# Kernel optimization log

Measured on AMD Instinct MI355X. Metric: run time of the kernel, lower is better.

## Reference

```python
import jax, jax.numpy as jnp
import numpy as np

B, N, C, HID, NC = 8, 2000, 4096, 42, 20
THRESH = 0.5
EPS = 1e-12


def setup_inputs() -> dict:
    key = jax.random.key(0)
    ks = jax.random.split(key, 10)
    x1 = jax.random.normal(ks[0], (B, N, C), dtype=jnp.float32)
    x2 = jax.random.normal(ks[1], (B * N, 32), dtype=jnp.float32)  # unused after pooling in original
    xy = jax.random.uniform(ks[2], (B, N, 2), minval=0.0, maxval=800.0)
    wh = jax.random.uniform(ks[3], (B, N, 2), minval=20.0, maxval=300.0)
    boxes = jnp.concatenate([xy, xy + wh], axis=-1).astype(jnp.float32)  # [B,N,4] x1y1x2y2

    def lin(k, fi, fo):
        return (jax.random.normal(k, (fi, fo), jnp.float32) / np.sqrt(fi)).astype(jnp.float32)

    return {
        'x1': x1, 'x2': x2, 'boxes': boxes,
        'W_cls1': lin(ks[4], C, HID), 'b_cls1': jnp.zeros((HID,), jnp.float32),
        'W_cls2': lin(ks[5], HID, NC), 'b_cls2': jnp.zeros((NC,), jnp.float32),
        'W_det1': lin(ks[6], C, HID), 'b_det1': jnp.zeros((HID,), jnp.float32),
        'W_det2': lin(ks[7], HID, NC), 'b_det2': jnp.zeros((NC,), jnp.float32),
    }


def _pairwise_iou(b):  # b: [N,4]
    area = (b[:, 2] - b[:, 0]) * (b[:, 3] - b[:, 1])
    lt = jnp.maximum(b[:, None, :2], b[None, :, :2])
    rb = jnp.minimum(b[:, None, 2:], b[None, :, 2:])
    wh = jnp.clip(rb - lt, 0.0)
    inter = wh[..., 0] * wh[..., 1]
    union = area[:, None] + area[None, :] - inter
    return inter / jnp.maximum(union, EPS)


def _row_normalize(m):  # Kipf-style: D^-1 m, zero rows -> 0
    s = jnp.sum(m, axis=1, keepdims=True)
    inv = jnp.where(s == 0.0, 0.0, 1.0 / jnp.where(s == 0.0, 1.0, s))
    return m * inv


def _per_image(x, b, W_cls1, b_cls1, W_cls2, b_cls2, W_det1, b_det1, W_det2, b_det2):
    # adjacency graph from box IoU, thresholded at 0.5; edges are unweighted (GCNConv normalize=False)
    iou = _pairwise_iou(b)
    A_adj = (iou >= THRESH).astype(x.dtype)  # [N,N], includes diagonal (self-IoU=1)
    # similarity graph from cosine similarity of features
    sf = x / jnp.maximum(jnp.linalg.norm(x, axis=1, keepdims=True), EPS)
    sim = jnp.nan_to_num(sf @ sf.T)
    A_sim = (sim >= THRESH).astype(x.dtype)
    # features are detached + row-normalized in the original
    xn = _row_normalize(jax.lax.stop_gradient(x))
    # GCNConv(add_self_loops=False, normalize=False): out = A_bin @ (X @ W) + bias
    h = jax.nn.relu(A_adj @ (xn @ W_cls1) + b_cls1)  # dropout is identity in eval
    cls = A_adj @ (h @ W_cls2) + b_cls2
    hd = jax.nn.relu(A_sim @ (xn @ W_det1) + b_det1)
    det = A_sim @ (hd @ W_det2) + b_det2
    return cls, det  # [N,NC] each


def reference(x1, x2, boxes, W_cls1, b_cls1, W_cls2, b_cls2, W_det1, b_det1, W_det2, b_det2):
    # x2 is pooled then unused in the original forward
    cls, det = jax.vmap(_per_image, in_axes=(0, 0) + (None,) * 8)(
        x1, boxes, W_cls1, b_cls1, W_cls2, b_cls2, W_det1, b_det1, W_det2, b_det2)
    # eval-mode post-processing
    cls = jax.nn.softmax(cls, axis=-1)          # softmax over classes
    det = jax.nn.softmax(det, axis=1)           # per-image softmax over proposals (dim=0 per image)
    cls_logit = cls.reshape(B * N, NC)
    det_logit = det.reshape(B * N, NC)
    return cls_logit, det_logit
```

## Files before the change

kernel.cpp:

```cpp
#include <hip/hip_runtime.h>
#include <stdint.h>

typedef unsigned int u32;
typedef unsigned long long u64;
typedef unsigned short u16;
typedef unsigned char u8;

#define B_IMG 8
#define N_BOX 2000
#define N_PAD 2048
#define C_DIM 4096
#define HIDN 42
#define NCLS 20
#define NWRD 64
#define NPAIR 136
#define YG_STEPS 128

using f32x4 = __attribute__((ext_vector_type(4))) float;
using s16x8 = __attribute__((ext_vector_type(8))) short;

__device__ __forceinline__ u32 f2bf(float f) {
    u32 u = __float_as_uint(f);
    u += 0x7FFFu + ((u >> 16) & 1u);
    return u >> 16;
}

#define GLOAD_LDS16(g, l)                                                     \
    __builtin_amdgcn_global_load_lds(                                         \
        (const __attribute__((address_space(1))) void*)(g),                   \
        (__attribute__((address_space(3))) void*)(l), 16, 0, 0)

__global__ __launch_bounds__(256) void wt_build(const float* __restrict__ Wc,
                                                const float* __restrict__ Wd,
                                                u16* __restrict__ Wth,
                                                u16* __restrict__ Wtl) {
    int g = blockIdx.x * 256 + threadIdx.x;
    if (g >= 96 * C_DIM) return;
    int k = g & (C_DIM - 1);
    int c = g >> 12;
    float v = 0.0f;
    if (c < HIDN) v = Wc[k * HIDN + c];
    else if (c < 2 * HIDN) v = Wd[k * HIDN + (c - HIDN)];
    u32 hb = f2bf(v);
    float hf = __uint_as_float(hb << 16);
    u32 lb = f2bf(v - hf);
    Wth[g] = (u16)hb;
    Wtl[g] = (u16)lb;
}

__global__ __launch_bounds__(256) void sf_pad(u8* __restrict__ SF,
                                              float* __restrict__ NRM) {
    int row = blockIdx.x;
    int img = row / 48, n = N_BOX + row % 48;
    uint4* p = (uint4*)(SF + ((size_t)img * N_PAD + n) * C_DIM);
    uint4 z = make_uint4(0, 0, 0, 0);
    p[threadIdx.x] = z;
    if (threadIdx.x == 0) NRM[(size_t)img * N_PAD + n] = 1e9f;
}

__global__ __launch_bounds__(256) void rowstats(const float* __restrict__ x,
                                                float* __restrict__ inv_sum,
                                                u8* __restrict__ sf,
                                                float* __restrict__ nrm) {
    int r = blockIdx.x;
    int t = threadIdx.x;
    u8* sfrow = sf + (size_t)r * C_DIM;
    if (r >= N_BOX) {
        uint4 z = make_uint4(0, 0, 0, 0);
        uint4* p = (uint4*)sfrow;
        for (int i = t; i < C_DIM / 16; i += 256) p[i] = z;
        if (t == 0) nrm[r] = 1e9f;
        return;
    }
    const float4* xr = (const float4*)(x + (size_t)r * C_DIM);
    float4 v[4];
    float s = 0.0f, ss = 0.0f;
#pragma unroll
    for (int i = 0; i < 4; i++) {
        v[i] = xr[t + 256 * i];
        s += v[i].x + v[i].y + v[i].z + v[i].w;
        ss += v[i].x * v[i].x + v[i].y * v[i].y + v[i].z * v[i].z + v[i].w * v[i].w;
    }
    __shared__ float red[4][2];
#pragma unroll
    for (int off = 32; off; off >>= 1) {
        s += __shfl_down(s, off);
        ss += __shfl_down(ss, off);
    }
    int wid = t >> 6, lane = t & 63;
    if (lane == 0) { red[wid][0] = s; red[wid][1] = ss; }
    __syncthreads();
    s  = red[0][0] + red[1][0] + red[2][0] + red[3][0];
    ss = red[0][1] + red[1][1] + red[2][1] + red[3][1];
    if (t == 0) {
        inv_sum[r] = (s == 0.0f) ? 0.0f : 1.0f / s;
        nrm[r] = sqrtf(ss);
    }
    u32* sp = (u32*)sfrow;
#pragma unroll
    for (int i = 0; i < 4; i++) {
        float4 w = v[i];
        u32 pk = __builtin_amdgcn_cvt_pk_fp8_f32(4.f * w.x, 4.f * w.y, 0, false);
        pk = __builtin_amdgcn_cvt_pk_fp8_f32(4.f * w.z, 4.f * w.w, pk, true);
        sp[t + 256 * i] = pk;
    }
}

__global__ __launch_bounds__(256) void gemm_sim(const u8* __restrict__ sf_all,
                                                const float* __restrict__ nrm_all,
                                                u32* __restrict__ bits_all) {
    __shared__ __align__(16) char smem[32768];
    char* tmat = smem;

    int z = blockIdx.z;
    const u8* sf = sf_all + (size_t)z * N_PAD * C_DIM;
    const float* nrm = nrm_all + (size_t)z * N_PAD;
    u32* bits = bits_all + (size_t)z * N_PAD * NWRD;

    int p = blockIdx.x;
    int bi = (int)((sqrtf(8.0f * p + 1.0f) - 1.0f) * 0.5f);
    while (bi * (bi + 1) / 2 > p) bi--;
    while ((bi + 1) * (bi + 2) / 2 <= p) bi++;
    int bj = p - bi * (bi + 1) / 2;

    int t = threadIdx.x;
    int lane = t & 63;
    int w = t >> 6;
    int wm = w >> 1, wn = w & 1;
    int tr0 = bi * 128, tc0 = bj * 128;
    f32x4 acc[4][4] = {};
    int q = lane & 15, g = lane >> 4;
    int swz = (q >> 1) & 3;
    int g8 = (g & 1) * 8, gh = g >> 1;

    auto stage = [&](int it, int b) {
        int k0 = it * 64;
        u8* As = (u8*)smem + b * 16384;
        u8* Bs = As + 8192;
#pragma unroll
        for (int i = 0; i < 2; i++) {
            int ci = t + 256 * i;
            int r = ci >> 2, c16 = ci & 3;
            int sc16 = c16 ^ ((r >> 1) & 3);
            GLOAD_LDS16(sf + ((size_t)(tr0 + r) << 12) + k0 + sc16 * 16,
                        As + ci * 16);
            GLOAD_LDS16(sf + ((size_t)(tc0 + r) << 12) + k0 + sc16 * 16,
                        Bs + ci * 16);
        }
    };

    stage(0, 0);
    __syncthreads();
    for (int it = 0; it < 64; ++it) {
        int cur = it & 1;
        if (it + 1 < 64) stage(it + 1, cur ^ 1);
        const u8* As = (const u8*)smem + cur * 16384;
        const u8* Bs = As + 8192;
#pragma unroll
        for (int kk = 0; kk < 2; kk++) {
            int boff = ((2 * kk + gh) ^ swz) * 16 + g8;
            long long a[4], b[4];
#pragma unroll
            for (int m = 0; m < 4; m++)
                a[m] = *(const long long*)(As + (wm * 64 + m * 16 + q) * 64 + boff);
#pragma unroll
            for (int n = 0; n < 4; n++)
                b[n] = *(const long long*)(Bs + (wn * 64 + n * 16 + q) * 64 + boff);
#pragma unroll
            for (int m = 0; m < 4; m++)
#pragma unroll
                for (int n = 0; n < 4; n++)
                    acc[m][n] = __builtin_amdgcn_mfma_f32_16x16x32_fp8_fp8(a[m], b[n], acc[m][n], 0, 0, 0);
        }
        __syncthreads();
    }

    float ncol[4];
#pragma unroll
    for (int n = 0; n < 4; n++) ncol[n] = nrm[tc0 + wn * 64 + n * 16 + q];
#pragma unroll
    for (int m = 0; m < 4; m++)
#pragma unroll
        for (int j = 0; j < 4; j++) {
            int row = wm * 64 + m * 16 + g * 4 + j;
            float thr8 = 8.0f * nrm[tr0 + row];
#pragma unroll
            for (int n = 0; n < 4; n++) {
                int col = wn * 64 + n * 16 + q;
                tmat[row * 132 + col] = (acc[m][n][j] >= thr8 * ncol[n]) ? 1 : 0;
            }
        }
    __syncthreads();

    for (int rr = 0; rr < 32; rr++) {
        int row = w * 32 + rr;
#pragma unroll
        for (int h = 0; h < 2; h++) {
            u64 b = __ballot(tmat[row * 132 + h * 64 + lane] != 0);
            if (lane < 2)
                bits[(size_t)(tr0 + row) * NWRD + bj * 4 + 2 * h + lane] = (u32)(b >> (32 * lane));
        }
    }
    if (bi != bj) {
        for (int rr = 0; rr < 32; rr++) {
            int c = w * 32 + rr;
#pragma unroll
            for (int h = 0; h < 2; h++) {
                u64 b = __ballot(tmat[(h * 64 + lane) * 132 + c] != 0);
                if (lane < 2)
                    bits[(size_t)(tc0 + c) * NWRD + bi * 4 + 2 * h + lane] = (u32)(b >> (32 * lane));
            }
        }
    }
}

__global__ __launch_bounds__(256) void iou_bits(const float* __restrict__ boxes,
                                                u32* __restrict__ bits) {
    __shared__ float bx[N_BOX * 4];
    int blk = blockIdx.x;
    int img = blk / 500;
    int r0 = (blk % 500) * 4;
    const float* bb = boxes + (size_t)img * N_BOX * 4;
    for (int i = threadIdx.x; i < N_BOX * 4; i += 256) bx[i] = bb[i];
    __syncthreads();
    int t = threadIdx.x;
    int ri = r0 + (t >> 6);
    int wi = t & 63;
    float x1a = bx[ri * 4 + 0], y1a = bx[ri * 4 + 1];
    float x2a = bx[ri * 4 + 2], y2a = bx[ri * 4 + 3];
    float areaA = __fmul_rn(__fsub_rn(x2a, x1a), __fsub_rn(y2a, y1a));
    u32 wv = 0;
    int jb = wi * 32;
#pragma unroll 4
    for (int s = 0; s < 32; s++) {
        int j = jb + s;
        if (j < N_BOX) {
            float x1b = bx[j * 4 + 0], y1b = bx[j * 4 + 1];
            float x2b = bx[j * 4 + 2], y2b = bx[j * 4 + 3];
            float areaB = __fmul_rn(__fsub_rn(x2b, x1b), __fsub_rn(y2b, y1b));
            float ltx = fmaxf(x1a, x1b), lty = fmaxf(y1a, y1b);
            float rbx = fminf(x2a, x2b), rby = fminf(y2a, y2b);
            float wx = fmaxf(__fsub_rn(rbx, ltx), 0.0f);
            float wy = fmaxf(__fsub_rn(rby, lty), 0.0f);
            float inter = __fmul_rn(wx, wy);
            float uni = __fsub_rn(__fadd_rn(areaA, areaB), inter);
            float iou = __fdiv_rn(inter, fmaxf(uni, 1e-12f));
            if (iou >= 0.5f) wv |= (1u << s);
        }
    }
    bits[((size_t)img * N_PAD + ri) * NWRD + wi] = wv;
}

__global__ __launch_bounds__(256) void ygemm_fused(const float* __restrict__ x,
                                                   const u16* __restrict__ Wh,
                                                   const u16* __restrict__ Wl,
                                                   const float* __restrict__ INV,
                                                   u8* __restrict__ SF,
                                                   float* __restrict__ NRM,
                                                   float* __restrict__ Y,
                                                   int emit) {
    __shared__ u16 Ah[2][32 * 32];
    __shared__ u16 Al[2][32 * 32];
    __shared__ u16 Bh[2][96 * 32];
    __shared__ u16 Bl[2][96 * 32];
    __shared__ float invLds[32];

    int t = threadIdx.x;
    int row0 = blockIdx.x * 32;
    int ar = t >> 3;
    int grow = row0 + ar;
    int img = grow / N_BOX, nrow = grow - img * N_BOX;
    size_t sf_off = ((size_t)img * N_PAD + nrow) * C_DIM + (t & 7) * 4;
    const float* xrow = x + (size_t)grow * C_DIM + (t & 7) * 4;

    int w = t >> 6, lane = t & 63;
    int q = lane & 15, g = lane >> 4;
    int wr = (w & 1) * 16, wc = (w >> 1) * 48;

    f32x4 acc[3] = {};
    float sum = 0.0f, ssq = 0.0f;

    auto stage_B = [&](int sstep, int b) {
        int ks = sstep * 32;
#pragma unroll
        for (int i = 0; i < 3; i++) {
            int idx = t + 256 * i;
            int half = idx >= 384;
            int loc = half ? idx - 384 : idx;
            int cr = loc >> 2, kc2 = loc & 3;
            const u16* src = (half ? Wl : Wh) + (size_t)cr * C_DIM + ks + kc2 * 8;
            u16* dst = (half ? Bl[b] : Bh[b]) + loc * 8;
            GLOAD_LDS16(src, dst);
        }
    };

    float4 pa = *(const float4*)(xrow);
    stage_B(0, 0);

    for (int s = 0; s < YG_STEPS; ++s) {
        int buf = s & 1;
        {
            float e[4] = {pa.x, pa.y, pa.z, pa.w};
            if (emit) {
                sum += e[0] + e[1] + e[2] + e[3];
                ssq += e[0] * e[0] + e[1] * e[1] + e[2] * e[2] + e[3] * e[3];
                u32 pk = __builtin_amdgcn_cvt_pk_fp8_f32(4.f * e[0], 4.f * e[1], 0, false);
                pk = __builtin_amdgcn_cvt_pk_fp8_f32(4.f * e[2], 4.f * e[3], pk, true);
                *(u32*)(SF + sf_off + (size_t)s * 32) = pk;
            }
            u32 hb[4], lb[4];
#pragma unroll
            for (int j = 0; j < 4; j++) {
                hb[j] = f2bf(e[j]);
                float hf = __uint_as_float(hb[j] << 16);
                lb[j] = f2bf(e[j] - hf);
            }
            *(uint2*)&Ah[buf][t * 4] = make_uint2(hb[0] | (hb[1] << 16), hb[2] | (hb[3] << 16));
            *(uint2*)&Al[buf][t * 4] = make_uint2(lb[0] | (lb[1] << 16), lb[2] | (lb[3] << 16));
        }
        __syncthreads();
        if (s + 1 < YG_STEPS) {
            stage_B(s + 1, buf ^ 1);
            pa = *(const float4*)(xrow + (s + 1) * 32);
        }
        s16x8 fah, fal, fbh[3], fbl[3];
        fah = *(const s16x8*)&Ah[buf][(wr + q) * 32 + g * 8];
        fal = *(const s16x8*)&Al[buf][(wr + q) * 32 + g * 8];
#pragma unroll
        for (int n = 0; n < 3; n++) {
            fbh[n] = *(const s16x8*)&Bh[buf][(wc + n * 16 + q) * 32 + g * 8];
            fbl[n] = *(const s16x8*)&Bl[buf][(wc + n * 16 + q) * 32 + g * 8];
        }
#pragma unroll
        for (int n = 0; n < 3; n++) {
            acc[n] = __builtin_amdgcn_mfma_f32_16x16x32_bf16(fah, fbh[n], acc[n], 0, 0, 0);
            acc[n] = __builtin_amdgcn_mfma_f32_16x16x32_bf16(fal, fbh[n], acc[n], 0, 0, 0);
            acc[n] = __builtin_amdgcn_mfma_f32_16x16x32_bf16(fah, fbl[n], acc[n], 0, 0, 0);
        }
    }

    if (emit) {
        sum += __shfl_xor(sum, 1); sum += __shfl_xor(sum, 2); sum += __shfl_xor(sum, 4);
        ssq += __shfl_xor(ssq, 1); ssq += __shfl_xor(ssq, 2); ssq += __shfl_xor(ssq, 4);
        if ((t & 7) == 0) {
            invLds[ar] = (sum == 0.0f) ? 0.0f : 1.0f / sum;
            NRM[(size_t)img * N_PAD + nrow] = sqrtf(ssq);
        }
    } else {
        if ((t & 7) == 0) invLds[ar] = INV[grow];
    }
    __syncthreads();

#pragma unroll
    for (int n = 0; n < 3; n++)
#pragma unroll
        for (int j = 0; j < 4; j++) {
            int lr = wr + g * 4 + j;
            int c = wc + n * 16 + q;
            Y[(size_t)(row0 + lr) * 96 + c] = acc[n][j] * invLds[lr];
        }
}

__global__ __launch_bounds__(256) void spmm1(const u32* __restrict__ Aadj,
                                             const u32* __restrict__ Asim,
                                             const float* __restrict__ Y,
                                             const float* __restrict__ bc1,
                                             const float* __restrict__ bd1,
                                             float* __restrict__ H) {
    int gw = blockIdx.x * 4 + (threadIdx.x >> 6);
    int lane = threadIdx.x & 63;
    if (lane >= HIDN) return;
    int i = gw >> 1, br = gw & 1;
    int img = i / N_BOX, n = i % N_BOX;
    const u32* bp = (br ? Asim : Aadj) + ((size_t)img * N_PAD + n) * NWRD;
    const float* Yb = Y + (size_t)img * N_BOX * 96 + br * HIDN + lane;
    float acc = 0.0f;
    for (int w8 = 0; w8 < NWRD; w8++) {
        u32 wv = bp[w8];
        while (wv) {
            int s = __builtin_ctz(wv);
            wv &= wv - 1;
            acc += Yb[(size_t)(w8 * 32 + s) * 96];
        }
    }
    float bias = br ? bd1[lane] : bc1[lane];
    H[(size_t)i * 96 + br * HIDN + lane] = fmaxf(acc + bias, 0.0f);
}

__global__ __launch_bounds__(256) void gemm2(const float* __restrict__ H,
                                             const float* __restrict__ Wc2,
                                             const float* __restrict__ Wd2,
                                             float* __restrict__ Z) {
    __shared__ float w2[2 * HIDN * NCLS];
    for (int idx = threadIdx.x; idx < 2 * HIDN * NCLS; idx += 256) {
        int br = idx / (HIDN * NCLS), e = idx % (HIDN * NCLS);
        w2[idx] = br ? Wd2[e] : Wc2[e];
    }
    __syncthreads();
    int gidx = blockIdx.x * 256 + threadIdx.x;
    if (gidx >= 16000 * 40) return;
    int i = gidx / 40, rem = gidx % 40;
    int br = rem / NCLS, c2 = rem % NCLS;
    const float* hrow = H + (size_t)i * 96 + br * HIDN;
    const float* wp = w2 + br * HIDN * NCLS;
    float acc = 0.0f;
#pragma unroll
    for (int h = 0; h < HIDN; h++) acc += hrow[h] * wp[h * NCLS + c2];
    Z[gidx] = acc;
}

__global__ __launch_bounds__(256) void spmm2(const u32* __restrict__ Aadj,
                                             const u32* __restrict__ Asim,
                                             const float* __restrict__ Z,
                                             const float* __restrict__ bc2,
                                             const float* __restrict__ bd2,
                                             float* __restrict__ out) {
    int gw = blockIdx.x * 4 + (threadIdx.x >> 6);
    int lane = threadIdx.x & 63;
    if (lane >= NCLS) return;
    int i = gw >> 1, br = gw & 1;
    int img = i / N_BOX, n = i % N_BOX;
    const u32* bp = (br ? Asim : Aadj) + ((size_t)img * N_PAD + n) * NWRD;
    const float* Zb = Z + (size_t)img * N_BOX * 40 + br * NCLS + lane;
    float acc = 0.0f;
    for (int w8 = 0; w8 < NWRD; w8++) {
        u32 wv = bp[w8];
        while (wv) {
            int s = __builtin_ctz(wv);
            wv &= wv - 1;
            acc += Zb[(size_t)(w8 * 32 + s) * 40];
        }
    }
    float logit = acc + (br ? bd2[lane] : bc2[lane]);
    out[(br ? 320000 : 0) + (size_t)i * NCLS + lane] = logit;
}

__global__ __launch_bounds__(256) void softmax_cls(float* __restrict__ out) {
    int i = blockIdx.x * 256 + threadIdx.x;
    if (i >= 16000) return;
    float* p = out + (size_t)i * NCLS;
    float m = p[0];
#pragma unroll
    for (int c = 1; c < NCLS; c++) m = fmaxf(m, p[c]);
    float e[NCLS], s = 0.0f;
#pragma unroll
    for (int c = 0; c < NCLS; c++) { e[c] = expf(p[c] - m); s += e[c]; }
    float inv = 1.0f / s;
#pragma unroll
    for (int c = 0; c < NCLS; c++) p[c] = e[c] * inv;
}

__global__ __launch_bounds__(256) void softmax_det(float* __restrict__ out) {
    __shared__ float vals[N_BOX];
    __shared__ float redm[4];
    __shared__ float reds[4];
    int img = blockIdx.x / NCLS, c = blockIdx.x % NCLS;
    float* base = out + 320000 + (size_t)img * N_BOX * NCLS + c;
    int t = threadIdx.x;
    float m = -3.4e38f;
    for (int n = t; n < N_BOX; n += 256) {
        float v = base[(size_t)n * NCLS];
        vals[n] = v;
        m = fmaxf(m, v);
    }
#pragma unroll
    for (int off = 32; off; off >>= 1) m = fmaxf(m, __shfl_down(m, off));
    if ((t & 63) == 0) redm[t >> 6] = m;
    __syncthreads();
    m = fmaxf(fmaxf(redm[0], redm[1]), fmaxf(redm[2], redm[3]));
    float s = 0.0f;
    for (int n = t; n < N_BOX; n += 256) s += expf(vals[n] - m);
#pragma unroll
    for (int off = 32; off; off >>= 1) s += __shfl_down(s, off);
    if ((t & 63) == 0) reds[t >> 6] = s;
    __syncthreads();
    s = reds[0] + reds[1] + reds[2] + reds[3];
    float inv = 1.0f / s;
    for (int n = t; n < N_BOX; n += 256) base[(size_t)n * NCLS] = expf(vals[n] - m) * inv;
}

extern "C" void kernel_launch(void* const* d_in, const int* in_sizes, int n_in,
                              void* d_out, int out_size, void* d_ws, size_t ws_size,
                              hipStream_t stream) {
    const float* x1    = (const float*)d_in[0];
    const float* boxes = (const float*)d_in[2];
    const float* W_cls1 = (const float*)d_in[3];
    const float* b_cls1 = (const float*)d_in[4];
    const float* W_cls2 = (const float*)d_in[5];
    const float* b_cls2 = (const float*)d_in[6];
    const float* W_det1 = (const float*)d_in[7];
    const float* b_det1 = (const float*)d_in[8];
    const float* W_det2 = (const float*)d_in[9];
    const float* b_det2 = (const float*)d_in[10];
    float* out = (float*)d_out;

    char* ws = (char*)d_ws;
    size_t off = 0;
    auto alloc = [&](size_t bytes) -> void* {
        void* p = ws + off;
        off = (off + bytes + 255) & ~(size_t)255;
        return p;
    };
    u16* WTH   = (u16*)alloc((size_t)96 * C_DIM * 2);
    u16* WTL   = (u16*)alloc((size_t)96 * C_DIM * 2);
    float* INV = (float*)alloc((size_t)16000 * 4);
    float* NRM = (float*)alloc((size_t)B_IMG * N_PAD * 4);
    u32* AADJ  = (u32*)alloc((size_t)B_IMG * N_PAD * NWRD * 4);
    u32* ASIM  = (u32*)alloc((size_t)B_IMG * N_PAD * NWRD * 4);
    float* Y   = (float*)alloc((size_t)16000 * 96 * 4);
    float* H   = (float*)alloc((size_t)16000 * 96 * 4);
    float* Z   = (float*)alloc((size_t)16000 * 40 * 4);
    size_t base_need = off;
    size_t sf_full = (size_t)B_IMG * N_PAD * C_DIM;
    bool full = (ws_size >= base_need + sf_full);
    u8* SF = (u8*)alloc(full ? sf_full : (size_t)N_PAD * C_DIM);

    wt_build<<<dim3(1536), dim3(256), 0, stream>>>(W_cls1, W_det1, WTH, WTL);
    iou_bits<<<dim3(B_IMG * 500), dim3(256), 0, stream>>>(boxes, AADJ);

    if (full) {
        sf_pad<<<dim3(B_IMG * 48), dim3(256), 0, stream>>>(SF, NRM);
        ygemm_fused<<<dim3(500), dim3(256), 0, stream>>>(x1, WTH, WTL, INV, SF, NRM, Y, 1);
        gemm_sim<<<dim3(NPAIR, 1, B_IMG), dim3(256), 0, stream>>>(SF, NRM, ASIM);
    } else {
        for (int b = 0; b < B_IMG; b++) {
            rowstats<<<dim3(N_PAD), dim3(256), 0, stream>>>(
                x1 + (size_t)b * N_BOX * C_DIM, INV + (size_t)b * N_BOX, SF,
                NRM + (size_t)b * N_PAD);
            gemm_sim<<<dim3(NPAIR, 1, 1), dim3(256), 0, stream>>>(
                SF, NRM + (size_t)b * N_PAD, ASIM + (size_t)b * N_PAD * NWRD);
        }
        ygemm_fused<<<dim3(500), dim3(256), 0, stream>>>(x1, WTH, WTL, INV, SF, NRM, Y, 0);
    }

    spmm1<<<dim3(8000), dim3(256), 0, stream>>>(AADJ, ASIM, Y, b_cls1, b_det1, H);
    gemm2<<<dim3(2500), dim3(256), 0, stream>>>(H, W_cls2, W_det2, Z);
    spmm2<<<dim3(8000), dim3(256), 0, stream>>>(AADJ, ASIM, Z, b_cls2, b_det2, out);
    softmax_cls<<<dim3(63), dim3(256), 0, stream>>>(out);
    softmax_det<<<dim3(160), dim3(256), 0, stream>>>(out);
    (void)in_sizes; (void)n_in; (void)out_size; (void)d_in; (void)ws_size;
}
```

Before: 536.2 us.

## Rewrite ygemm as single-wave blocks with register-prefetched operands, no LDS

The Y = X·W GEMM kernel is restructured from 256-thread blocks that stage A and B through double-buffered LDS with a barrier each step into 64-thread single-wave blocks, each computing 16 rows by all 96 columns. The A fragments are converted to bf16 hi/lo directly in registers from global loads that are prefetched four steps ahead. The W fragments are loaded straight from global memory into registers with one-step double buffering. This removes the LDS traffic and __syncthreads and deepens the x-load pipeline, at the cost of much higher register pressure and every wave re-reading W from L2 instead of sharing it through LDS.

```diff
diff --git a/kernel.cpp b/kernel.cpp
--- a/kernel.cpp
+++ b/kernel.cpp
@@ -251,114 +251,100 @@
     bits[((size_t)img * N_PAD + ri) * NWRD + wi] = wv;
 }
 
-__global__ __launch_bounds__(256) void ygemm_fused(const float* __restrict__ x,
-                                                   const u16* __restrict__ Wh,
-                                                   const u16* __restrict__ Wl,
-                                                   const float* __restrict__ INV,
-                                                   u8* __restrict__ SF,
-                                                   float* __restrict__ NRM,
-                                                   float* __restrict__ Y,
-                                                   int emit) {
-    __shared__ u16 Ah[2][32 * 32];
-    __shared__ u16 Al[2][32 * 32];
-    __shared__ u16 Bh[2][96 * 32];
-    __shared__ u16 Bl[2][96 * 32];
-    __shared__ float invLds[32];
-
-    int t = threadIdx.x;
-    int row0 = blockIdx.x * 32;
-    int ar = t >> 3;
-    int grow = row0 + ar;
+#define YG_LOADW(ks, WH_, WL_)                                                \
+    _Pragma("unroll")                                                         \
+    for (int n = 0; n < 6; n++) {                                             \
+        int col = n * 16 + q;                                                 \
+        WH_[n] = *(const s16x8*)(Wh + (size_t)col * C_DIM + (ks) + g * 8);    \
+        WL_[n] = *(const s16x8*)(Wl + (size_t)col * C_DIM + (ks) + g * 8);    \
+    }
+
+#define YG_STEP(sidx, d, CH, CL, NH, NL)                                      \
+    {                                                                         \
+        int s_ = (sidx);                                                      \
+        if (s_ + 1 < YG_STEPS) { YG_LOADW((s_ + 1) * 32, NH, NL) }            \
+        float4 a0 = xa[d][0], a1 = xa[d][1];                                  \
+        if (s_ + 4 < YG_STEPS) {                                              \
+            xa[d][0] = *(const float4*)(xp + (s_ + 4) * 32);                  \
+            xa[d][1] = *(const float4*)(xp + (s_ + 4) * 32 + 4);              \
+        }                                                                     \
+        float e[8] = {a0.x, a0.y, a0.z, a0.w, a1.x, a1.y, a1.z, a1.w};        \
+        if (emit) {                                                           \
+            sum += e[0] + e[1] + e[2] + e[3] + e[4] + e[5] + e[6] + e[7];     \
+            ssq += e[0]*e[0] + e[1]*e[1] + e[2]*e[2] + e[3]*e[3] +            \
+                   e[4]*e[4] + e[5]*e[5] + e[6]*e[6] + e[7]*e[7];             \
+            u32 lo = __builtin_amdgcn_cvt_pk_fp8_f32(4.f*e[0], 4.f*e[1], 0, false); \
+            lo = __builtin_amdgcn_cvt_pk_fp8_f32(4.f*e[2], 4.f*e[3], lo, true);     \
+            u32 hi = __builtin_amdgcn_cvt_pk_fp8_f32(4.f*e[4], 4.f*e[5], 0, false); \
+            hi = __builtin_amdgcn_cvt_pk_fp8_f32(4.f*e[6], 4.f*e[7], hi, true);     \
+            *(uint2*)(sfp + (size_t)s_ * 32) = make_uint2(lo, hi);            \
+        }                                                                     \
+        s16x8 fah, fal;                                                       \
+        _Pragma("unroll")                                                     \
+        for (int j2 = 0; j2 < 8; j2++) {                                      \
+            u32 hb = f2bf(e[j2]);                                             \
+            float hf = __uint_as_float(hb << 16);                             \
+            fah[j2] = (short)hb;                                              \
+            fal[j2] = (short)f2bf(e[j2] - hf);                                \
+        }                                                                     \
+        _Pragma("unroll")                                                     \
+        for (int n = 0; n < 6; n++) {                                         \
+            acc[n] = __builtin_amdgcn_mfma_f32_16x16x32_bf16(fah, CH[n], acc[n], 0, 0, 0); \
+            acc[n] = __builtin_amdgcn_mfma_f32_16x16x32_bf16(fal, CH[n], acc[n], 0, 0, 0); \
+            acc[n] = __builtin_amdgcn_mfma_f32_16x16x32_bf16(fah, CL[n], acc[n], 0, 0, 0); \
+        }                                                                     \
+    }
+
+__global__ __launch_bounds__(64) void ygemm_fused(const float* __restrict__ x,
+                                                  const u16* __restrict__ Wh,
+                                                  const u16* __restrict__ Wl,
+                                                  const float* __restrict__ INV,
+                                                  u8* __restrict__ SF,
+                                                  float* __restrict__ NRM,
+                                                  float* __restrict__ Y,
+                                                  int emit) {
+    int lane = threadIdx.x;
+    int q = lane & 15, g = lane >> 4;
+    int row0 = blockIdx.x * 16;
+    int grow = row0 + q;
     int img = grow / N_BOX, nrow = grow - img * N_BOX;
-    size_t sf_off = ((size_t)img * N_PAD + nrow) * C_DIM + (t & 7) * 4;
-    const float* xrow = x + (size_t)grow * C_DIM + (t & 7) * 4;
-
-    int w = t >> 6, lane = t & 63;
-    int q = lane & 15, g = lane >> 4;
-    int wr = (w & 1) * 16, wc = (w >> 1) * 48;
-
-    f32x4 acc[3] = {};
+    const float* xp = x + (size_t)grow * C_DIM + g * 8;
+    u8* sfp = SF + ((size_t)img * N_PAD + nrow) * C_DIM + g * 8;
+
+    f32x4 acc[6] = {};
     float sum = 0.0f, ssq = 0.0f;
 
-    auto stage_B = [&](int sstep, int b) {
-        int ks = sstep * 32;
-#pragma unroll
-        for (int i = 0; i < 3; i++) {
-            int idx = t + 256 * i;
-            int half = idx >= 384;
-            int loc = half ? idx - 384 : idx;
-            int cr = loc >> 2, kc2 = loc & 3;
-            const u16* src = (half ? Wl : Wh) + (size_t)cr * C_DIM + ks + kc2 * 8;
-            u16* dst = (half ? Bl[b] : Bh[b]) + loc * 8;
-            GLOAD_LDS16(src, dst);
-        }
-    };
-
-    float4 pa = *(const float4*)(xrow);
-    stage_B(0, 0);
-
-    for (int s = 0; s < YG_STEPS; ++s) {
-        int buf = s & 1;
-        {
-            float e[4] = {pa.x, pa.y, pa.z, pa.w};
-            if (emit) {
-                sum += e[0] + e[1] + e[2] + e[3];
-                ssq += e[0] * e[0] + e[1] * e[1] + e[2] * e[2] + e[3] * e[3];
-                u32 pk = __builtin_amdgcn_cvt_pk_fp8_f32(4.f * e[0], 4.f * e[1], 0, false);
-                pk = __builtin_amdgcn_cvt_pk_fp8_f32(4.f * e[2], 4.f * e[3], pk, true);
-                *(u32*)(SF + sf_off + (size_t)s * 32) = pk;
-            }
-            u32 hb[4], lb[4];
-#pragma unroll
-            for (int j = 0; j < 4; j++) {
-                hb[j] = f2bf(e[j]);
-                float hf = __uint_as_float(hb[j] << 16);
-                lb[j] = f2bf(e[j] - hf);
-            }
-            *(uint2*)&Ah[buf][t * 4] = make_uint2(hb[0] | (hb[1] << 16), hb[2] | (hb[3] << 16));
-            *(uint2*)&Al[buf][t * 4] = make_uint2(lb[0] | (lb[1] << 16), lb[2] | (lb[3] << 16));
-        }
-        __syncthreads();
-        if (s + 1 < YG_STEPS) {
-            stage_B(s + 1, buf ^ 1);
-            pa = *(const float4*)(xrow + (s + 1) * 32);
-        }
-        s16x8 fah, fal, fbh[3], fbl[3];
-        fah = *(const s16x8*)&Ah[buf][(wr + q) * 32 + g * 8];
-        fal = *(const s16x8*)&Al[buf][(wr + q) * 32 + g * 8];
-#pragma unroll
-        for (int n = 0; n < 3; n++) {
-            fbh[n] = *(const s16x8*)&Bh[buf][(wc + n * 16 + q) * 32 + g * 8];
-            fbl[n] = *(const s16x8*)&Bl[buf][(wc + n * 16 + q) * 32 + g * 8];
-        }
-#pragma unroll
-        for (int n = 0; n < 3; n++) {
-            acc[n] = __builtin_amdgcn_mfma_f32_16x16x32_bf16(fah, fbh[n], acc[n], 0, 0, 0);
-            acc[n] = __builtin_amdgcn_mfma_f32_16x16x32_bf16(fal, fbh[n], acc[n], 0, 0, 0);
-            acc[n] = __builtin_amdgcn_mfma_f32_16x16x32_bf16(fah, fbl[n], acc[n], 0, 0, 0);
-        }
-    }
-
+    float4 xa[4][2];
+#pragma unroll
+    for (int d = 0; d < 4; d++) {
+        xa[d][0] = *(const float4*)(xp + d * 32);
+        xa[d][1] = *(const float4*)(xp + d * 32 + 4);
+    }
+    s16x8 wAh[6], wAl[6], wBh[6], wBl[6];
+    YG_LOADW(0, wAh, wAl)
+
+#pragma unroll 1
+    for (int so = 0; so < 32; ++so) {
+        YG_STEP(so * 4 + 0, 0, wAh, wAl, wBh, wBl)
+        YG_STEP(so * 4 + 1, 1, wBh, wBl, wAh, wAl)
+        YG_STEP(so * 4 + 2, 2, wAh, wAl, wBh, wBl)
+        YG_STEP(so * 4 + 3, 3, wBh, wBl, wAh, wAl)
+    }
+
+    float inv = 0.0f;
     if (emit) {
-        sum += __shfl_xor(sum, 1); sum += __shfl_xor(sum, 2); sum += __shfl_xor(sum, 4);
-        ssq += __shfl_xor(ssq, 1); ssq += __shfl_xor(ssq, 2); ssq += __shfl_xor(ssq, 4);
-        if ((t & 7) == 0) {
-            invLds[ar] = (sum == 0.0f) ? 0.0f : 1.0f / sum;
-            NRM[(size_t)img * N_PAD + nrow] = sqrtf(ssq);
-        }
-    } else {
-        if ((t & 7) == 0) invLds[ar] = INV[grow];
-    }
-    __syncthreads();
-
-#pragma unroll
-    for (int n = 0; n < 3; n++)
-#pragma unroll
-        for (int j = 0; j < 4; j++) {
-            int lr = wr + g * 4 + j;
-            int c = wc + n * 16 + q;
-            Y[(size_t)(row0 + lr) * 96 + c] = acc[n][j] * invLds[lr];
-        }
+        sum += __shfl_xor(sum, 16); sum += __shfl_xor(sum, 32);
+        ssq += __shfl_xor(ssq, 16); ssq += __shfl_xor(ssq, 32);
+        inv = (sum == 0.0f) ? 0.0f : 1.0f / sum;
+        if (g == 0) NRM[(size_t)img * N_PAD + nrow] = sqrtf(ssq);
+    }
+#pragma unroll
+    for (int j = 0; j < 4; j++) {
+        float invr = emit ? __shfl(inv, g * 4 + j) : INV[row0 + g * 4 + j];
+#pragma unroll
+        for (int n = 0; n < 6; n++)
+            Y[(size_t)(row0 + g * 4 + j) * 96 + n * 16 + q] = acc[n][j] * invr;
+    }
 }
 
 __global__ __launch_bounds__(256) void spmm1(const u32* __restrict__ Aadj,
@@ -520,7 +506,7 @@
 
     if (full) {
         sf_pad<<<dim3(B_IMG * 48), dim3(256), 0, stream>>>(SF, NRM);
-        ygemm_fused<<<dim3(500), dim3(256), 0, stream>>>(x1, WTH, WTL, INV, SF, NRM, Y, 1);
+        ygemm_fused<<<dim3(1000), dim3(64), 0, stream>>>(x1, WTH, WTL, INV, SF, NRM, Y, 1);
         gemm_sim<<<dim3(NPAIR, 1, B_IMG), dim3(256), 0, stream>>>(SF, NRM, ASIM);
     } else {
         for (int b = 0; b < B_IMG; b++) {
@@ -530,7 +516,7 @@
             gemm_sim<<<dim3(NPAIR, 1, 1), dim3(256), 0, stream>>>(
                 SF, NRM + (size_t)b * N_PAD, ASIM + (size_t)b * N_PAD * NWRD);
         }
-        ygemm_fused<<<dim3(500), dim3(256), 0, stream>>>(x1, WTH, WTL, INV, SF, NRM, Y, 0);
+        ygemm_fused<<<dim3(1000), dim3(64), 0, stream>>>(x1, WTH, WTL, INV, SF, NRM, Y, 0);
     }
 
     spmm1<<<dim3(8000), dim3(256), 0, stream>>>(AADJ, ASIM, Y, b_cls1, b_det1, H);
```

Measured after the change: 589.8 us. 10.0% more time.
